# Kernel tuning notes

Measured on AMD Instinct MI355X. Metric: run time of the kernel, lower is better.

## Reference

```python
import jax, jax.numpy as jnp
import numpy as np

P = 40000       # points
DEG = 16        # neighbors per point (bs_slice rows are full: count == DEG)
E = P * DEG     # total edges
CI = 16         # in channels
CO = 16         # out channels


def setup_inputs() -> dict:
    key = jax.random.key(0)
    k1, k2, k3, k4 = jax.random.split(key, 4)
    features = jax.random.normal(k1, (P, CI), dtype=jnp.float32)
    radii = jax.random.normal(k2, (E, 3), dtype=jnp.float32)
    W = jax.random.normal(k3, (3, CO, CI), dtype=jnp.float32) * 0.1
    # bs_slice: [P, 1+DEG]; col 0 = neighbor count (DEG), cols 1: = neighbor idx
    nbrs = jax.random.randint(k4, (P, DEG), 0, P, dtype=jnp.int32)
    counts = jnp.full((P, 1), DEG, dtype=jnp.int32)
    bs_slice = jnp.concatenate([counts, nbrs], axis=1)
    return {"features": features, "radii": radii, "W": W, "bs_slice": bs_slice}


def reference(features, radii, W, bs_slice):
    # Edge list: torch loop consumes kernels sequentially, point-major.
    points_num = features.shape[0]
    deg = bs_slice.shape[1] - 1
    fa = jnp.repeat(jnp.arange(points_num, dtype=jnp.int32), deg)   # [E] dest point
    fb = bs_slice[:, 1:].reshape(-1)                                # [E] src point
    # Kernel(radii): linear radial map -> per-edge kernel [E, CO, CI]
    kernels = jnp.einsum('ed,doi->eoi', radii, W)
    # message per edge: kernels[e] @ features[fb[e]]
    msg = jnp.einsum('eoi,ei->eo', kernels, features[fb])
    # scatter-add into destination points
    out = jax.ops.segment_sum(msg, fa, num_segments=points_num)     # [P, CO]
    return out
```

## Files before the change

### kernel.cpp

```cpp
#include <hip/hip_runtime.h>


__global__ __launch_bounds__(256) void k_conv(const float* __restrict__ feat,
                                              const float* __restrict__ radii,
                                              const float* __restrict__ W,
                                              const int* __restrict__ bs,
                                              float* __restrict__ out,
                                              int P) {
    __shared__ __align__(16) float s_Wt[16][52];
    __shared__ __align__(16) int   s_nbr[16][16];
    __shared__ __align__(16) float s_r[16][48];
    __shared__ __align__(16) float s_h[16][48];

    const int tid = threadIdx.x;
    const int pbase = blockIdx.x * 16;
    const int lp = tid >> 4;
    const int li = tid & 15;

    for (int t = tid; t < 768; t += 256) {
        const int d = t >> 8, o = (t >> 4) & 15, i = t & 15;
        s_Wt[o][d * 16 + i] = W[t];
    }
    {
        const int p = pbase + lp;
        s_nbr[lp][li] = (p < P) ? bs[(size_t)p * 17 + 1 + li] : 0;
    }
    if (tid < 192) {
        const size_t gi4  = (size_t)pbase * 12 + tid;
        const size_t lim4 = (size_t)P * 12;
        float4 v = {0.f, 0.f, 0.f, 0.f};
        if (gi4 < lim4) v = reinterpret_cast<const float4*>(radii)[gi4];
        reinterpret_cast<float4*>(&s_r[0][0])[tid] = v;
    }
    __syncthreads();

    int nb[16];
    {
        const int4* nb4 = reinterpret_cast<const int4*>(&s_nbr[lp][0]);
#pragma unroll
        for (int j = 0; j < 4; ++j) {
            const int4 v = nb4[j];
            nb[j*4+0] = v.x; nb[j*4+1] = v.y; nb[j*4+2] = v.z; nb[j*4+3] = v.w;
        }
    }
    float r[48];
    {
        const float4* r4 = reinterpret_cast<const float4*>(&s_r[lp][0]);
#pragma unroll
        for (int j = 0; j < 12; ++j) {
            const float4 v = r4[j];
            r[j*4+0] = v.x; r[j*4+1] = v.y; r[j*4+2] = v.z; r[j*4+3] = v.w;
        }
    }

    float h0 = 0.f, h1 = 0.f, h2 = 0.f;
#pragma unroll
    for (int n = 0; n < 16; ++n) {
        const float fv = feat[((size_t)nb[n] << 4) + li];
        h0 += r[n * 3 + 0] * fv;
        h1 += r[n * 3 + 1] * fv;
        h2 += r[n * 3 + 2] * fv;
    }
    s_h[lp][li]      = h0;
    s_h[lp][16 + li] = h1;
    s_h[lp][32 + li] = h2;
    __syncthreads();

    float acc = 0.f;
    {
        const float4* w4 = reinterpret_cast<const float4*>(&s_Wt[li][0]);
        const float4* h4 = reinterpret_cast<const float4*>(&s_h[lp][0]);
#pragma unroll
        for (int j = 0; j < 12; ++j) {
            const float4 w = w4[j];
            const float4 h = h4[j];
            acc += w.x * h.x + w.y * h.y + w.z * h.z + w.w * h.w;
        }
    }
    const int p = pbase + lp;
    if (p < P) out[(size_t)p * 16 + li] = acc;
}

extern "C" void kernel_launch(void* const* d_in, const int* in_sizes, int n_in,
                              void* d_out, int out_size, void* d_ws, size_t ws_size,
                              hipStream_t stream) {
    const float* feat  = (const float*)d_in[0];
    const float* radii = (const float*)d_in[1];
    const float* W     = (const float*)d_in[2];
    const int*   bs    = (const int*)d_in[3];
    float* out = (float*)d_out;

    const int P = in_sizes[0] / 16;
    const int grid = (P + 15) / 16;
    k_conv<<<grid, 256, 0, stream>>>(feat, radii, W, bs, out, P);
}
```

Measured before the change: 12.31 us.

## Load radii directly to registers and reduce output via shuffle transpose-reduce

Removes the shared-memory staging of radii and the per-point intermediate h buffer, along with the second __syncthreads. Each thread now reads its point's 48 radii directly from global memory as float4s. The final 16x48 W contraction becomes per-lane partial products over all 16 outputs, combined by a butterfly shuffle reduce-scatter across the 16 lanes. The W layout in shared memory is transposed to suit this. The cost is redundant radii loads (16 lanes read the same row, relying on cache) and extra register pressure plus shuffle work.

```diff
diff --git a/kernel.cpp b/kernel.cpp
--- a/kernel.cpp
+++ b/kernel.cpp
@@ -9,8 +9,6 @@
                                               int P) {
     __shared__ __align__(16) float s_Wt[16][52];
     __shared__ __align__(16) int   s_nbr[16][16];
-    __shared__ __align__(16) float s_r[16][48];
-    __shared__ __align__(16) float s_h[16][48];
 
     const int tid = threadIdx.x;
     const int pbase = blockIdx.x * 16;
@@ -19,21 +17,26 @@
 
     for (int t = tid; t < 768; t += 256) {
         const int d = t >> 8, o = (t >> 4) & 15, i = t & 15;
-        s_Wt[o][d * 16 + i] = W[t];
+        s_Wt[i][d * 16 + o] = W[t];
     }
     {
         const int p = pbase + lp;
         s_nbr[lp][li] = (p < P) ? bs[(size_t)p * 17 + 1 + li] : 0;
     }
-    if (tid < 192) {
-        const size_t gi4  = (size_t)pbase * 12 + tid;
-        const size_t lim4 = (size_t)P * 12;
-        float4 v = {0.f, 0.f, 0.f, 0.f};
-        if (gi4 < lim4) v = reinterpret_cast<const float4*>(radii)[gi4];
-        reinterpret_cast<float4*>(&s_r[0][0])[tid] = v;
-    }
     __syncthreads();
 
+    const int p = pbase + lp;
+    if (p >= P) return;
+
+    float rr[48];
+    {
+        const float4* r4 = reinterpret_cast<const float4*>(radii + (size_t)p * 48);
+#pragma unroll
+        for (int j = 0; j < 12; ++j) {
+            const float4 v = r4[j];
+            rr[j*4+0] = v.x; rr[j*4+1] = v.y; rr[j*4+2] = v.z; rr[j*4+3] = v.w;
+        }
+    }
     int nb[16];
     {
         const int4* nb4 = reinterpret_cast<const int4*>(&s_nbr[lp][0]);
@@ -43,42 +46,67 @@
             nb[j*4+0] = v.x; nb[j*4+1] = v.y; nb[j*4+2] = v.z; nb[j*4+3] = v.w;
         }
     }
-    float r[48];
-    {
-        const float4* r4 = reinterpret_cast<const float4*>(&s_r[lp][0]);
-#pragma unroll
-        for (int j = 0; j < 12; ++j) {
-            const float4 v = r4[j];
-            r[j*4+0] = v.x; r[j*4+1] = v.y; r[j*4+2] = v.z; r[j*4+3] = v.w;
-        }
-    }
 
     float h0 = 0.f, h1 = 0.f, h2 = 0.f;
 #pragma unroll
     for (int n = 0; n < 16; ++n) {
         const float fv = feat[((size_t)nb[n] << 4) + li];
-        h0 += r[n * 3 + 0] * fv;
-        h1 += r[n * 3 + 1] * fv;
-        h2 += r[n * 3 + 2] * fv;
+        h0 += rr[n*3+0] * fv;
+        h1 += rr[n*3+1] * fv;
+        h2 += rr[n*3+2] * fv;
     }
-    s_h[lp][li]      = h0;
-    s_h[lp][16 + li] = h1;
-    s_h[lp][32 + li] = h2;
-    __syncthreads();
 
-    float acc = 0.f;
+    float po[16];
     {
         const float4* w4 = reinterpret_cast<const float4*>(&s_Wt[li][0]);
-        const float4* h4 = reinterpret_cast<const float4*>(&s_h[lp][0]);
 #pragma unroll
-        for (int j = 0; j < 12; ++j) {
+        for (int j = 0; j < 4; ++j) {
             const float4 w = w4[j];
-            const float4 h = h4[j];
-            acc += w.x * h.x + w.y * h.y + w.z * h.z + w.w * h.w;
+            po[j*4+0] = w.x*h0; po[j*4+1] = w.y*h0; po[j*4+2] = w.z*h0; po[j*4+3] = w.w*h0;
+        }
+#pragma unroll
+        for (int j = 0; j < 4; ++j) {
+            const float4 w = w4[4+j];
+            po[j*4+0] += w.x*h1; po[j*4+1] += w.y*h1; po[j*4+2] += w.z*h1; po[j*4+3] += w.w*h1;
+        }
+#pragma unroll
+        for (int j = 0; j < 4; ++j) {
+            const float4 w = w4[8+j];
+            po[j*4+0] += w.x*h2; po[j*4+1] += w.y*h2; po[j*4+2] += w.z*h2; po[j*4+3] += w.w*h2;
         }
     }
-    const int p = pbase + lp;
-    if (p < P) out[(size_t)p * 16 + li] = acc;
+
+    const bool b8 = (li & 8) != 0;
+    float v8[8];
+#pragma unroll
+    for (int k = 0; k < 8; ++k) {
+        const float send = b8 ? po[k] : po[k+8];
+        const float keep = b8 ? po[k+8] : po[k];
+        v8[k] = keep + __shfl_xor(send, 8, 16);
+    }
+    const bool b4 = (li & 4) != 0;
+    float v4[4];
+#pragma unroll
+    for (int k = 0; k < 4; ++k) {
+        const float send = b4 ? v8[k] : v8[k+4];
+        const float keep = b4 ? v8[k+4] : v8[k];
+        v4[k] = keep + __shfl_xor(send, 4, 16);
+    }
+    const bool b2 = (li & 2) != 0;
+    float v2[2];
+#pragma unroll
+    for (int k = 0; k < 2; ++k) {
+        const float send = b2 ? v4[k] : v4[k+2];
+        const float keep = b2 ? v4[k+2] : v4[k];
+        v2[k] = keep + __shfl_xor(send, 2, 16);
+    }
+    const bool b1 = (li & 1) != 0;
+    {
+        const float send = b1 ? v2[0] : v2[1];
+        const float keep = b1 ? v2[1] : v2[0];
+        const float res = keep + __shfl_xor(send, 1, 16);
+        out[(size_t)p * 16 + li] = res;
+    }
 }
 
 extern "C" void kernel_launch(void* const* d_in, const int* in_sizes, int n_in,
```

Measured after the change: 14.21 us. 15.4% more time.
